# Kernel optimization log

Measured on AMD Instinct MI355X. Metric: run time of the kernel, lower is better.

## Reference

```python
import math
import jax, jax.numpy as jnp
import numpy as np

B, N = 1, 512
C_S, C_Z, H, C, P_Q, P_V = 384, 128, 12, 16, 4, 8
CAT = C_Z * H + C * H + 3 * H * P_V + 1  # 2017


def _apply(t_r, t_t, x):
    # t_r: (b,n,3,3), t_t: (b,n,3), x: (b,3,h,p,n) -> global frame coords
    xg = jnp.einsum('bnij,bjhpn->bihpn', t_r, x)
    return xg + jnp.swapaxes(t_t, 1, 2)[:, :, None, None, :]


def setup_inputs() -> dict:
    key = jax.random.key(0)
    ks = jax.random.split(key, 14)
    f = lambda k, shp: jax.random.normal(k, shp, dtype=jnp.float32)
    return {
        's': f(ks[0], (B, C_S, N)),
        'z': f(ks[1], (B, C_Z, N, N)),
        't_r': f(ks[2], (B, N, 3, 3)),
        't_t': f(ks[3], (B, N, 3)),
        'Wq': f(ks[4], (C * H, C_S)) * 0.02,
        'Wk': f(ks[5], (C * H, C_S)) * 0.02,
        'Wv': f(ks[6], (C * H, C_S)) * 0.02,
        'Wqp': f(ks[7], (3 * H * P_Q, C_S)) * 0.02,
        'Wkp': f(ks[8], (3 * H * P_Q, C_S)) * 0.02,
        'Wvp': f(ks[9], (3 * H * P_V, C_S)) * 0.02,
        'Wb': f(ks[10], (H, C_Z)) * 0.02,
        'gamma': f(ks[11], (H, 1, 1)) * 0.5,
        'Ws': f(ks[12], (C_S, CAT)) * 0.02,
        'bs': jnp.zeros((C_S,), dtype=jnp.float32),
    }


def reference(s, z, t_r, t_t, Wq, Wk, Wv, Wqp, Wkp, Wvp, Wb, gamma, Ws, bs):
    b, _, n = s.shape
    w_c = math.sqrt(2.0 / (9.0 * P_Q))
    w_l = math.sqrt(1.0 / 3.0)

    proj = lambda W: jnp.einsum('oc,bcn->bon', W, s)
    # torch rearrange 'b (c h) i -> b c h i' == reshape(b, c, h, n)
    q = proj(Wq).reshape(b, C, H, n)
    k = proj(Wk).reshape(b, C, H, n)
    v = proj(Wv).reshape(b, C, H, n)
    qp = proj(Wqp).reshape(b, 3, H, P_Q, n)
    kp = proj(Wkp).reshape(b, 3, H, P_Q, n)
    vp = proj(Wvp).reshape(b, 3, H, P_V, n)

    qg = _apply(t_r, t_t, qp)  # (b,3,h,p,n)
    kg = _apply(t_r, t_t, kp)
    diff = qg[..., :, None] - kg[..., None, :]          # (b,3,h,p,n,n)
    dist2 = jnp.sum(diff * diff, axis=(1, 3))           # sum coords + points -> (b,h,n,n)
    tmp = jax.nn.softplus(gamma)[None] * (w_c / 2.0) * dist2

    b_bias = jnp.einsum('hc,bcij->bhij', Wb, z)
    qk = jnp.einsum('bchi,bchj->bhij', q, k) / math.sqrt(C)
    a = jax.nn.softmax(w_l * (qk + b_bias - tmp), axis=-1)  # (b,h,n,n)

    o1 = jnp.einsum('bhij,bcij->bchi', a, z).reshape(b, C_Z * H, n)
    o2 = jnp.einsum('bhij,bchj->bchi', a, v).reshape(b, C * H, n)

    vg = _apply(t_r, t_t, vp)                           # (b,3,h,pv,n)
    o3g = jnp.einsum('bhij,bchpj->bchpi', a, vg)        # (b,3,h,pv,n)
    t_r_inv = jnp.swapaxes(t_r, -1, -2)
    t_t_inv = jnp.einsum('bnij,bnj->bni', -t_r_inv, t_t)
    o3 = _apply(t_r_inv, t_t_inv, o3g).reshape(b, 3 * H * P_V, n)
    o3_norm = jnp.linalg.norm(o3, axis=1, keepdims=True)  # (b,1,n)

    cat = jnp.concatenate([o1, o2, o3, o3_norm], axis=1)  # (b, CAT, n)
    return jnp.einsum('oc,bcn->bon', Ws, cat) + bs[None, :, None]
```

## Files before the change

### kernel.cpp

```cpp
#include <hip/hip_runtime.h>
#include <math.h>

#define N 512
#define H 12
#define CC 16
#define CZ 128
#define CS 384
#define PQ 4
#define PV 8
#define CATR 2017

__global__ __launch_bounds__(256) void k_proj(
    const float* __restrict__ s,
    const float* __restrict__ Wq, const float* __restrict__ Wk, const float* __restrict__ Wv,
    const float* __restrict__ Wqp, const float* __restrict__ Wkp, const float* __restrict__ Wvp,
    float* __restrict__ proj)
{
    __shared__ float Wt[16][33];
    __shared__ float St[32][128];
    int t = threadIdx.x;
    int o0 = blockIdx.x * 16;
    int n0 = blockIdx.y * 128;
    const float* Wsrc; int orow;
    if (o0 < 192)      { Wsrc = Wq;  orow = o0; }
    else if (o0 < 384) { Wsrc = Wk;  orow = o0-192; }
    else if (o0 < 576) { Wsrc = Wv;  orow = o0-384; }
    else if (o0 < 720) { Wsrc = Wqp; orow = o0-576; }
    else if (o0 < 864) { Wsrc = Wkp; orow = o0-720; }
    else               { Wsrc = Wvp; orow = o0-864; }

    int og = t >> 6, nl = t & 63;
    float acc[4][2] = {};
    for (int c0 = 0; c0 < CS; c0 += 32) {
        __syncthreads();
        for (int k = 0; k < 2; k++) {
            int idx = t + k*256;
            int oo = idx >> 5, ccol = idx & 31;
            Wt[oo][ccol] = Wsrc[(orow+oo)*CS + c0 + ccol];
        }
        for (int k = 0; k < 4; k++) {
            int idx = t + k*256;
            int ccr = idx >> 5, nn4 = idx & 31;
            float4 v = *(const float4*)&s[(c0+ccr)*N + n0 + nn4*4];
            *(float4*)&St[ccr][nn4*4] = v;
        }
        __syncthreads();
        for (int kk = 0; kk < 32; kk++) {
            float sv0 = St[kk][nl], sv1 = St[kk][nl+64];
            #pragma unroll
            for (int r = 0; r < 4; r++) {
                float w = Wt[og*4+r][kk];
                acc[r][0] += w * sv0;
                acc[r][1] += w * sv1;
            }
        }
    }
    for (int r = 0; r < 4; r++) {
        int o = o0 + og*4 + r;
        proj[o*N + n0 + nl]      = acc[r][0];
        proj[o*N + n0 + 64 + nl] = acc[r][1];
    }
}

__global__ void k_frames(const float* __restrict__ proj,
                         const float* __restrict__ t_r, const float* __restrict__ t_t,
                         float* __restrict__ qg, float* __restrict__ kg, float* __restrict__ vg)
{
    int gid = blockIdx.x * blockDim.x + threadIdx.x;
    int n = gid & (N-1);
    int hp = gid >> 9;
    if (hp >= 192) return;
    const float* src; float* dst; int rowb, stride;
    if (hp < 48)      { src = proj + 576*N; dst = qg; rowb = hp;    stride = 48; }
    else if (hp < 96) { src = proj + 720*N; dst = kg; rowb = hp-48; stride = 48; }
    else              { src = proj + 864*N; dst = vg; rowb = hp-96; stride = 96; }
    float x0 = src[(rowb + 0*stride)*N + n];
    float x1 = src[(rowb + 1*stride)*N + n];
    float x2 = src[(rowb + 2*stride)*N + n];
    #pragma unroll
    for (int d = 0; d < 3; d++) {
        float r0 = t_r[(n*3+d)*3+0], r1 = t_r[(n*3+d)*3+1], r2 = t_r[(n*3+d)*3+2];
        dst[(rowb + d*stride)*N + n] = r0*x0 + r1*x1 + r2*x2 + t_t[n*3+d];
    }
}

__global__ void k_sq(const float* __restrict__ qg, const float* __restrict__ kg,
                     float* __restrict__ sq_q, float* __restrict__ sq_k)
{
    int gid = blockIdx.x * blockDim.x + threadIdx.x;
    int n = gid & (N-1);
    int sel = gid >> 9;
    int h = sel % H;
    const float* g = (sel < H) ? qg : kg;
    float* outp = (sel < H) ? sq_q : sq_k;
    float acc = 0.f;
    #pragma unroll
    for (int d = 0; d < 3; d++)
        #pragma unroll
        for (int p = 0; p < PQ; p++) {
            float v = g[(size_t)((d*H + h)*PQ + p)*N + n];
            acc += v*v;
        }
    outp[h*N + n] = acc;
}

__global__ __launch_bounds__(256) void k_attn_o1(
    const float* __restrict__ z, const float* __restrict__ proj,
    const float* __restrict__ qg, const float* __restrict__ kg,
    const float* __restrict__ sq_q, const float* __restrict__ sq_k,
    const float* __restrict__ Wb, const float* __restrict__ gamma,
    float* __restrict__ a, float* __restrict__ cat)
{
    __shared__ float als[12*516];
    __shared__ float zls[128*68];
    int i = blockIdx.x;
    int t = threadIdx.x;
    int jl = t & 63;
    int cgu = __builtin_amdgcn_readfirstlane(t >> 6);
    const size_t NN = (size_t)N*N;
    const float w_l  = 0.57735026918962584f;
    const float w_c2 = 0.11785113019775793f;

    float ch[12];
    #pragma unroll
    for (int h = 0; h < 12; h++) {
        float g = gamma[h];
        float sp = (g > 20.f) ? g : log1pf(expf(g));
        ch[h] = sp * w_c2;
    }

    for (int jc = 0; jc < 2; jc++) {
        int j = jc*256 + jl*4;
        float acc[12][4] = {};

        {
            const float* zp = z + (size_t)(cgu*32)*NN + (size_t)i*N + j;
            for (int cc = 0; cc < 32; cc += 8) {
                float4 zb[8];
                #pragma unroll
                for (int u = 0; u < 8; u++)
                    zb[u] = *(const float4*)(zp + (size_t)(cc+u)*NN);
                #pragma unroll
                for (int u = 0; u < 8; u++) {
                    int c = cgu*32 + cc + u;
                    #pragma unroll
                    for (int h = 0; h < 12; h++) {
                        float w = Wb[h*CZ + c];
                        acc[h][0] += w*zb[u].x; acc[h][1] += w*zb[u].y;
                        acc[h][2] += w*zb[u].z; acc[h][3] += w*zb[u].w;
                    }
                }
            }
        }
        {
            const float* q  = proj;
            const float* kk = proj + 192*N;
            #pragma unroll
            for (int cc = 0; cc < 4; cc++) {
                int c = cgu*4 + cc;
                #pragma unroll
                for (int h = 0; h < 12; h++) {
                    int r = c*12 + h;
                    float qv = 0.25f * q[(size_t)r*N + i];
                    float4 k4 = *(const float4*)&kk[(size_t)r*N + j];
                    acc[h][0] += qv*k4.x; acc[h][1] += qv*k4.y;
                    acc[h][2] += qv*k4.z; acc[h][3] += qv*k4.w;
                }
            }
        }
        {
            #pragma unroll
            for (int dd = 0; dd < 3; dd++) {
                int dp = cgu*3 + dd; int d = dp >> 2, p = dp & 3;
                #pragma unroll
                for (int h = 0; h < 12; h++) {
                    int r = (d*12 + h)*4 + p;
                    float qv = 2.f * ch[h] * qg[(size_t)r*N + i];
                    float4 k4 = *(const float4*)&kg[(size_t)r*N + j];
                    acc[h][0] += qv*k4.x; acc[h][1] += qv*k4.y;
                    acc[h][2] += qv*k4.z; acc[h][3] += qv*k4.w;
                }
            }
        }

        __syncthreads();
        float* red = zls;
        if (cgu >= 2) {
            #pragma unroll
            for (int h = 0; h < 12; h++) {
                float4 v; v.x=acc[h][0]; v.y=acc[h][1]; v.z=acc[h][2]; v.w=acc[h][3];
                *(float4*)&red[(h*2 + (cgu-2))*256 + jl*4] = v;
            }
        }
        __syncthreads();
        if (cgu < 2) {
            #pragma unroll
            for (int h = 0; h < 12; h++) {
                float4 o = *(const float4*)&red[(h*2 + cgu)*256 + jl*4];
                acc[h][0] += o.x; acc[h][1] += o.y; acc[h][2] += o.z; acc[h][3] += o.w;
            }
            if (cgu == 1) {
                #pragma unroll
                for (int h = 0; h < 12; h++) {
                    float4 v; v.x=acc[h][0]; v.y=acc[h][1]; v.z=acc[h][2]; v.w=acc[h][3];
                    *(float4*)&red[(h*2 + 1)*256 + jl*4] = v;
                }
            }
        }
        __syncthreads();
        if (cgu == 0) {
            #pragma unroll
            for (int h = 0; h < 12; h++) {
                float4 o = *(const float4*)&red[(h*2 + 1)*256 + jl*4];
                float s0 = sq_q[h*N + i];
                float4 sk = *(const float4*)&sq_k[h*N + j];
                float4 r;
                r.x = w_l*(acc[h][0] + o.x - ch[h]*(s0 + sk.x));
                r.y = w_l*(acc[h][1] + o.y - ch[h]*(s0 + sk.y));
                r.z = w_l*(acc[h][2] + o.z - ch[h]*(s0 + sk.z));
                r.w = w_l*(acc[h][3] + o.w - ch[h]*(s0 + sk.w));
                *(float4*)&als[h*516 + jc*256 + jl*4] = r;
            }
        }
    }
    __syncthreads();

    #pragma unroll
    for (int hh = 0; hh < 3; hh++) {
        int h = cgu*3 + hh;
        float* row = &als[h*516 + jl*8];
        float4 v0 = *(const float4*)row;
        float4 v1 = *(const float4*)(row+4);
        float m = fmaxf(fmaxf(fmaxf(v0.x,v0.y),fmaxf(v0.z,v0.w)),
                        fmaxf(fmaxf(v1.x,v1.y),fmaxf(v1.z,v1.w)));
        for (int s = 32; s > 0; s >>= 1) m = fmaxf(m, __shfl_xor(m, s));
        v0.x = __expf(v0.x-m); v0.y = __expf(v0.y-m);
        v0.z = __expf(v0.z-m); v0.w = __expf(v0.w-m);
        v1.x = __expf(v1.x-m); v1.y = __expf(v1.y-m);
        v1.z = __expf(v1.z-m); v1.w = __expf(v1.w-m);
        float sm = v0.x+v0.y+v0.z+v0.w+v1.x+v1.y+v1.z+v1.w;
        for (int s = 32; s > 0; s >>= 1) sm += __shfl_xor(sm, s);
        float inv = 1.f/sm;
        v0.x*=inv; v0.y*=inv; v0.z*=inv; v0.w*=inv;
        v1.x*=inv; v1.y*=inv; v1.z*=inv; v1.w*=inv;
        *(float4*)row = v0;
        *(float4*)(row+4) = v1;
        float* garow = &a[((size_t)h*N + i)*N + jl*8];
        *(float4*)garow = v0;
        *(float4*)(garow+4) = v1;
    }
    __syncthreads();

    int cg = t & 31, hg = (t>>5)&1, jq = t>>6;
    float acc[4][6] = {};
    for (int jc = 0; jc < 8; jc++) {
        __syncthreads();
        #pragma unroll
        for (int k = 0; k < 8; k++) {
            int idx = t + k*256;
            int c = idx >> 4, j4 = idx & 15;
            *(float4*)&zls[c*68 + j4*4] =
                *(const float4*)&z[((size_t)c*N + i)*N + jc*64 + j4*4];
        }
        __syncthreads();
        #pragma unroll
        for (int s = 0; s < 4; s++) {
            int jo = jq*16 + s*4;
            float4 a4[6];
            #pragma unroll
            for (int hh = 0; hh < 6; hh++)
                a4[hh] = *(const float4*)&als[(hg*6+hh)*516 + jc*64 + jo];
            #pragma unroll
            for (int r = 0; r < 4; r++) {
                float4 zz = *(const float4*)&zls[(cg + 32*r)*68 + jo];
                #pragma unroll
                for (int hh = 0; hh < 6; hh++)
                    acc[r][hh] += zz.x*a4[hh].x + zz.y*a4[hh].y
                                + zz.z*a4[hh].z + zz.w*a4[hh].w;
            }
        }
    }
    __syncthreads();
    if (jq >= 2) {
        float* rb = &zls[((jq-2)*128 + (t & 127))*25];
        #pragma unroll
        for (int r = 0; r < 4; r++)
            #pragma unroll
            for (int hh = 0; hh < 6; hh++) rb[r*6+hh] = acc[r][hh];
    }
    __syncthreads();
    if (jq < 2) {
        const float* rb = &zls[(jq*128 + (t & 127))*25];
        #pragma unroll
        for (int r = 0; r < 4; r++)
            #pragma unroll
            for (int hh = 0; hh < 6; hh++) acc[r][hh] += rb[r*6+hh];
        if (jq == 1) {
            float* rb2 = &als[(t & 63)*25];
            #pragma unroll
            for (int r = 0; r < 4; r++)
                #pragma unroll
                for (int hh = 0; hh < 6; hh++) rb2[r*6+hh] = acc[r][hh];
        }
    }
    __syncthreads();
    if (jq == 0) {
        const float* rb2 = &als[t*25];
        #pragma unroll
        for (int r = 0; r < 4; r++)
            #pragma unroll
            for (int hh = 0; hh < 6; hh++) {
                float v = acc[r][hh] + rb2[r*6+hh];
                int c = cg + 32*r;
                int h = hg*6 + hh;
                cat[(size_t)(c*H + h)*N + i] = v;
            }
    }
}

__global__ __launch_bounds__(256) void k_o2o3g(
    const float* __restrict__ a, const float* __restrict__ proj, const float* __restrict__ vg,
    float* __restrict__ cat, float* __restrict__ o3g)
{
    __shared__ float ats[8*132];
    __shared__ float vts[40*132];
    int h = blockIdx.x, i0 = blockIdx.y*8;
    int t = threadIdx.x;
    int il = t & 7, rg = (t>>3)&7, jq = t>>6;
    const float* v = proj + 384*N;
    float acc[5] = {};
    for (int jc = 0; jc < 4; jc++) {
        __syncthreads();
        {
            int ii = t >> 5, j4 = t & 31;
            *(float4*)&ats[ii*132 + j4*4] =
                *(const float4*)&a[((size_t)h*N + i0+ii)*N + jc*128 + j4*4];
        }
        #pragma unroll
        for (int k = 0; k < 5; k++) {
            int idx = t + k*256;
            int r = idx >> 5, j4 = idx & 31;
            const float* src = (r < 16) ? (v + (size_t)(r*H + h)*N)
                : (vg + (size_t)(((r-16)>>3)*96 + h*PV + ((r-16)&7))*N);
            *(float4*)&vts[r*132 + j4*4] = *(const float4*)&src[jc*128 + j4*4];
        }
        __syncthreads();
        #pragma unroll
        for (int s = 0; s < 8; s++) {
            int jo = jq*32 + s*4;
            float4 a4 = *(const float4*)&ats[il*132 + jo];
            #pragma unroll
            for (int r = 0; r < 5; r++) {
                float4 v4 = *(const float4*)&vts[(rg*5+r)*132 + jo];
                acc[r] += v4.x*a4.x + v4.y*a4.y + v4.z*a4.z + v4.w*a4.w;
            }
        }
    }
    __syncthreads();
    if (jq >= 2) {
        float* rb = &ats[((jq-2)*64 + (t & 63))*5];
        #pragma unroll
        for (int r = 0; r < 5; r++) rb[r] = acc[r];
    }
    __syncthreads();
    if (jq < 2) {
        const float* rb = &ats[(jq*64 + (t & 63))*5];
        #pragma unroll
        for (int r = 0; r < 5; r++) acc[r] += rb[r];
        if (jq == 1) {
            float* rb2 = &ats[640 + (t & 63)*5];
            #pragma unroll
            for (int r = 0; r < 5; r++) rb2[r] = acc[r];
        }
    }
    __syncthreads();
    if (jq == 0) {
        const float* rb2 = &ats[640 + t*5];
        #pragma unroll
        for (int r = 0; r < 5; r++) {
            float val = acc[r] + rb2[r];
            int row = rg*5 + r;
            if (row < 16) cat[(size_t)(1536 + row*H + h)*N + i0 + il] = val;
            else { int rr = row - 16;
                   o3g[(size_t)((rr>>3)*96 + h*PV + (rr&7))*N + i0 + il] = val; }
        }
    }
}

__global__ void k_o3(const float* __restrict__ o3g,
                     const float* __restrict__ t_r, const float* __restrict__ t_t,
                     float* __restrict__ cat)
{
    int gid = blockIdx.x*blockDim.x + threadIdx.x;
    int i = gid & (N-1), hp = gid >> 9;
    if (hp >= 96) return;
    float x0 = o3g[(size_t)(0*96 + hp)*N + i] - t_t[i*3+0];
    float x1 = o3g[(size_t)(1*96 + hp)*N + i] - t_t[i*3+1];
    float x2 = o3g[(size_t)(2*96 + hp)*N + i] - t_t[i*3+2];
    #pragma unroll
    for (int d = 0; d < 3; d++) {
        float o = t_r[(i*3+0)*3+d]*x0 + t_r[(i*3+1)*3+d]*x1 + t_r[(i*3+2)*3+d]*x2;
        cat[(size_t)(1728 + d*96 + hp)*N + i] = o;
    }
}

__global__ void k_norm(float* __restrict__ cat)
{
    int i = blockIdx.x*blockDim.x + threadIdx.x;
    if (i >= N) return;
    float acc = 0.f;
    for (int r = 0; r < 288; r++) {
        float v = cat[(size_t)(1728+r)*N + i];
        acc += v*v;
    }
    cat[(size_t)2016*N + i] = sqrtf(acc);
}

__global__ __launch_bounds__(256) void k_final(
    const float* __restrict__ Ws, const float* __restrict__ bs,
    const float* __restrict__ cat, float* __restrict__ out)
{
    __shared__ float Wt[16*33];
    __shared__ float Ct[32*66];
    int o0 = blockIdx.x*16, n0 = blockIdx.y*64;
    int ks = blockIdx.z;
    int kbeg = ks*505, kend = min(CATR, kbeg+505);
    int t = threadIdx.x;
    int og = t >> 6, nl = t & 63;
    float acc[4] = {};
    for (int c0 = kbeg; c0 < kend; c0 += 32) {
        __syncthreads();
        for (int k = 0; k < 2; k++) {
            int idx = t + k*256;
            int oo = idx >> 5, ccol = idx & 31;
            int c = c0 + ccol;
            Wt[oo*33 + ccol] = (c < kend) ? Ws[(size_t)(o0+oo)*CATR + c] : 0.f;
        }
        for (int k = 0; k < 4; k++) {
            int idx = t + k*256;
            int ccr = idx >> 5, j2 = idx & 31;
            int c = c0 + ccr;
            float2 vv; vv.x = 0.f; vv.y = 0.f;
            if (c < kend) vv = *(const float2*)&cat[(size_t)c*N + n0 + j2*2];
            *(float2*)&Ct[ccr*66 + j2*2] = vv;
        }
        __syncthreads();
        int klim = min(32, kend - c0);
        for (int kk = 0; kk < klim; kk++) {
            float cv = Ct[kk*66 + nl];
            #pragma unroll
            for (int r = 0; r < 4; r++)
                acc[r] += Wt[(og*4+r)*33 + kk] * cv;
        }
    }
    #pragma unroll
    for (int r = 0; r < 4; r++) {
        int o = o0 + og*4 + r;
        float val = acc[r];
        if (ks == 0) val += bs[o];
        atomicAdd(&out[(size_t)o*N + n0 + nl], val);
    }
}

extern "C" void kernel_launch(void* const* d_in, const int* in_sizes, int n_in,
                              void* d_out, int out_size, void* d_ws, size_t ws_size,
                              hipStream_t stream)
{
    const float* s     = (const float*)d_in[0];
    const float* z     = (const float*)d_in[1];
    const float* t_r   = (const float*)d_in[2];
    const float* t_t   = (const float*)d_in[3];
    const float* Wq    = (const float*)d_in[4];
    const float* Wk    = (const float*)d_in[5];
    const float* Wv    = (const float*)d_in[6];
    const float* Wqp   = (const float*)d_in[7];
    const float* Wkp   = (const float*)d_in[8];
    const float* Wvp   = (const float*)d_in[9];
    const float* Wb    = (const float*)d_in[10];
    const float* gamma = (const float*)d_in[11];
    const float* Ws    = (const float*)d_in[12];
    const float* bs    = (const float*)d_in[13];
    float* out = (float*)d_out;

    float* ws   = (float*)d_ws;
    float* proj = ws;
    float* qg   = proj + 1152*N;
    float* kg   = qg   + 144*N;
    float* vg   = kg   + 144*N;
    float* sq_q = vg   + 288*N;
    float* sq_k = sq_q + H*N;
    float* o3g  = sq_k + H*N;
    float* a    = o3g  + 288*N;
    float* cat  = a    + (size_t)H*N*N;

    k_proj   <<<dim3(72,4),   256, 0, stream>>>(s, Wq, Wk, Wv, Wqp, Wkp, Wvp, proj);
    k_frames <<<384,          256, 0, stream>>>(proj, t_r, t_t, qg, kg, vg);
    k_sq     <<<48,           256, 0, stream>>>(qg, kg, sq_q, sq_k);
    k_attn_o1<<<512,          256, 0, stream>>>(z, proj, qg, kg, sq_q, sq_k, Wb, gamma, a, cat);
    k_o2o3g  <<<dim3(12,64),  256, 0, stream>>>(a, proj, vg, cat, o3g);
    k_o3     <<<192,          256, 0, stream>>>(o3g, t_r, t_t, cat);
    k_norm   <<<2,            256, 0, stream>>>(cat);
    hipMemsetAsync(out, 0, (size_t)CS*N*sizeof(float), stream);
    k_final  <<<dim3(24,8,4), 256, 0, stream>>>(Ws, bs, cat, out);
}
```

Measured before the change: 410.4 us.

## Split fused attention kernel into bias, softmax and o1 kernels with i-major logits

Replaces the single per-row kernel that computed logits, softmax and the z-weighted output into three kernels: a bias/logit kernel tiled over (i,j) blocks, a standalone softmax over a padded i-major logits buffer, and an o1 kernel that keeps attention rows in registers and streams z tiles through shared memory. The attention matrix is now stored as [i][h][j] with padded rows, and k_o2o3g reads that layout. The aim is better parallelism and occupancy than the 512-block fused kernel with its heavy shared memory and cross-wave reductions. In exchange, z is read twice from global memory and the logits take an extra global round trip.

```diff
diff --git a/kernel.cpp b/kernel.cpp
--- a/kernel.cpp
+++ b/kernel.cpp
@@ -9,6 +9,8 @@
 #define PQ 4
 #define PV 8
 #define CATR 2017
+#define ATROW 520
+#define ATPL  (H*ATROW)
 
 __global__ __launch_bounds__(256) void k_proj(
     const float* __restrict__ s,
@@ -104,22 +106,36 @@
     outp[h*N + n] = acc;
 }
 
-__global__ __launch_bounds__(256) void k_attn_o1(
+__global__ __launch_bounds__(128) void k_bias(
     const float* __restrict__ z, const float* __restrict__ proj,
     const float* __restrict__ qg, const float* __restrict__ kg,
     const float* __restrict__ sq_q, const float* __restrict__ sq_k,
     const float* __restrict__ Wb, const float* __restrict__ gamma,
-    float* __restrict__ a, float* __restrict__ cat)
-{
-    __shared__ float als[12*516];
-    __shared__ float zls[128*68];
-    int i = blockIdx.x;
+    float* __restrict__ a_t)
+{
+    __shared__ float q_ls[192*4];
+    __shared__ float qg_ls[144*4];
+    __shared__ float sqq_ls[12*4];
     int t = threadIdx.x;
-    int jl = t & 63;
-    int cgu = __builtin_amdgcn_readfirstlane(t >> 6);
+    int ii = t >> 5;
+    int jj = t & 31;
+    int i0 = blockIdx.x * 4;
+    int j0 = blockIdx.y * 128;
+    int i = i0 + ii;
+    int j4 = j0 + jj*4;
     const size_t NN = (size_t)N*N;
     const float w_l  = 0.57735026918962584f;
     const float w_c2 = 0.11785113019775793f;
+
+    for (int kk = 0; kk < 6; kk++) {
+        int idx = kk*128 + t;
+        if (idx < 768) { int r = idx >> 2, i2 = idx & 3; q_ls[idx] = proj[r*N + i0 + i2]; }
+    }
+    for (int kk = 0; kk < 5; kk++) {
+        int idx = kk*128 + t;
+        if (idx < 576) { int r = idx >> 2, i2 = idx & 3; qg_ls[idx] = qg[r*N + i0 + i2]; }
+    }
+    if (t < 48) { int r = t >> 2, i2 = t & 3; sqq_ls[t] = sq_q[r*N + i0 + i2]; }
 
     float ch[12];
     #pragma unroll
@@ -128,109 +144,68 @@
         float sp = (g > 20.f) ? g : log1pf(expf(g));
         ch[h] = sp * w_c2;
     }
-
-    for (int jc = 0; jc < 2; jc++) {
-        int j = jc*256 + jl*4;
-        float acc[12][4] = {};
-
-        {
-            const float* zp = z + (size_t)(cgu*32)*NN + (size_t)i*N + j;
-            for (int cc = 0; cc < 32; cc += 8) {
-                float4 zb[8];
-                #pragma unroll
-                for (int u = 0; u < 8; u++)
-                    zb[u] = *(const float4*)(zp + (size_t)(cc+u)*NN);
-                #pragma unroll
-                for (int u = 0; u < 8; u++) {
-                    int c = cgu*32 + cc + u;
-                    #pragma unroll
-                    for (int h = 0; h < 12; h++) {
-                        float w = Wb[h*CZ + c];
-                        acc[h][0] += w*zb[u].x; acc[h][1] += w*zb[u].y;
-                        acc[h][2] += w*zb[u].z; acc[h][3] += w*zb[u].w;
-                    }
-                }
+    __syncthreads();
+
+    float4 acc[12];
+    #pragma unroll
+    for (int h = 0; h < 12; h++) { acc[h].x=0.f; acc[h].y=0.f; acc[h].z=0.f; acc[h].w=0.f; }
+    for (int cb = 0; cb < CZ; cb += 8) {
+        float4 zb[8];
+        #pragma unroll
+        for (int u = 0; u < 8; u++)
+            zb[u] = *(const float4*)&z[(size_t)(cb+u)*NN + (size_t)i*N + j4];
+        #pragma unroll
+        for (int u = 0; u < 8; u++) {
+            int c = cb + u;
+            #pragma unroll
+            for (int h = 0; h < 12; h++) {
+                float w = Wb[h*CZ + c];
+                acc[h].x += w*zb[u].x; acc[h].y += w*zb[u].y;
+                acc[h].z += w*zb[u].z; acc[h].w += w*zb[u].w;
             }
         }
-        {
-            const float* q  = proj;
-            const float* kk = proj + 192*N;
-            #pragma unroll
-            for (int cc = 0; cc < 4; cc++) {
-                int c = cgu*4 + cc;
-                #pragma unroll
-                for (int h = 0; h < 12; h++) {
-                    int r = c*12 + h;
-                    float qv = 0.25f * q[(size_t)r*N + i];
-                    float4 k4 = *(const float4*)&kk[(size_t)r*N + j];
-                    acc[h][0] += qv*k4.x; acc[h][1] += qv*k4.y;
-                    acc[h][2] += qv*k4.z; acc[h][3] += qv*k4.w;
-                }
-            }
-        }
-        {
-            #pragma unroll
-            for (int dd = 0; dd < 3; dd++) {
-                int dp = cgu*3 + dd; int d = dp >> 2, p = dp & 3;
-                #pragma unroll
-                for (int h = 0; h < 12; h++) {
-                    int r = (d*12 + h)*4 + p;
-                    float qv = 2.f * ch[h] * qg[(size_t)r*N + i];
-                    float4 k4 = *(const float4*)&kg[(size_t)r*N + j];
-                    acc[h][0] += qv*k4.x; acc[h][1] += qv*k4.y;
-                    acc[h][2] += qv*k4.z; acc[h][3] += qv*k4.w;
-                }
-            }
-        }
-
-        __syncthreads();
-        float* red = zls;
-        if (cgu >= 2) {
-            #pragma unroll
-            for (int h = 0; h < 12; h++) {
-                float4 v; v.x=acc[h][0]; v.y=acc[h][1]; v.z=acc[h][2]; v.w=acc[h][3];
-                *(float4*)&red[(h*2 + (cgu-2))*256 + jl*4] = v;
-            }
-        }
-        __syncthreads();
-        if (cgu < 2) {
-            #pragma unroll
-            for (int h = 0; h < 12; h++) {
-                float4 o = *(const float4*)&red[(h*2 + cgu)*256 + jl*4];
-                acc[h][0] += o.x; acc[h][1] += o.y; acc[h][2] += o.z; acc[h][3] += o.w;
-            }
-            if (cgu == 1) {
-                #pragma unroll
-                for (int h = 0; h < 12; h++) {
-                    float4 v; v.x=acc[h][0]; v.y=acc[h][1]; v.z=acc[h][2]; v.w=acc[h][3];
-                    *(float4*)&red[(h*2 + 1)*256 + jl*4] = v;
-                }
-            }
-        }
-        __syncthreads();
-        if (cgu == 0) {
-            #pragma unroll
-            for (int h = 0; h < 12; h++) {
-                float4 o = *(const float4*)&red[(h*2 + 1)*256 + jl*4];
-                float s0 = sq_q[h*N + i];
-                float4 sk = *(const float4*)&sq_k[h*N + j];
-                float4 r;
-                r.x = w_l*(acc[h][0] + o.x - ch[h]*(s0 + sk.x));
-                r.y = w_l*(acc[h][1] + o.y - ch[h]*(s0 + sk.y));
-                r.z = w_l*(acc[h][2] + o.z - ch[h]*(s0 + sk.z));
-                r.w = w_l*(acc[h][3] + o.w - ch[h]*(s0 + sk.w));
-                *(float4*)&als[h*516 + jc*256 + jl*4] = r;
-            }
-        }
-    }
-    __syncthreads();
-
+    }
+
+    const float* kmat = proj + 192*N;
+    #pragma unroll
+    for (int h = 0; h < 12; h++) {
+        float4 qk; qk.x=0.f; qk.y=0.f; qk.z=0.f; qk.w=0.f;
+        #pragma unroll
+        for (int c = 0; c < 16; c++) {
+            int r = c*12 + h;
+            float  qs = q_ls[r*4 + ii];
+            float4 kv = *(const float4*)&kmat[(size_t)r*N + j4];
+            qk.x += qs*kv.x; qk.y += qs*kv.y; qk.z += qs*kv.z; qk.w += qs*kv.w;
+        }
+        float4 g4; g4.x=0.f; g4.y=0.f; g4.z=0.f; g4.w=0.f;
+        #pragma unroll
+        for (int dp = 0; dp < 12; dp++) {
+            int r = ((dp>>2)*12 + h)*4 + (dp&3);
+            float  qgs = qg_ls[r*4 + ii];
+            float4 kgv = *(const float4*)&kg[(size_t)r*N + j4];
+            g4.x += qgs*kgv.x; g4.y += qgs*kgv.y; g4.z += qgs*kgv.z; g4.w += qgs*kgv.w;
+        }
+        float  sqq = sqq_ls[h*4 + ii];
+        float4 sk  = *(const float4*)&sq_k[h*N + j4];
+        float4 l;
+        l.x = w_l*(acc[h].x + 0.25f*qk.x + ch[h]*(2.f*g4.x - sqq - sk.x));
+        l.y = w_l*(acc[h].y + 0.25f*qk.y + ch[h]*(2.f*g4.y - sqq - sk.y));
+        l.z = w_l*(acc[h].z + 0.25f*qk.z + ch[h]*(2.f*g4.z - sqq - sk.z));
+        l.w = w_l*(acc[h].w + 0.25f*qk.w + ch[h]*(2.f*g4.w - sqq - sk.w));
+        *(float4*)&a_t[(size_t)i*ATPL + h*ATROW + j4] = l;
+    }
+}
+
+__global__ __launch_bounds__(256) void k_softmax_t(float* __restrict__ a_t)
+{
+    int i = blockIdx.x;
+    int w = threadIdx.x >> 6, l = threadIdx.x & 63;
     #pragma unroll
     for (int hh = 0; hh < 3; hh++) {
-        int h = cgu*3 + hh;
-        float* row = &als[h*516 + jl*8];
+        int h = w*3 + hh;
+        float* row = a_t + (size_t)i*ATPL + h*ATROW + l*8;
         float4 v0 = *(const float4*)row;
-        float4 v1 = *(const float4*)(row+4);
+        float4 v1 = *(const float4*)(row + 4);
         float m = fmaxf(fmaxf(fmaxf(v0.x,v0.y),fmaxf(v0.z,v0.w)),
                         fmaxf(fmaxf(v1.x,v1.y),fmaxf(v1.z,v1.w)));
         for (int s = 32; s > 0; s >>= 1) m = fmaxf(m, __shfl_xor(m, s));
@@ -245,81 +220,68 @@
         v1.x*=inv; v1.y*=inv; v1.z*=inv; v1.w*=inv;
         *(float4*)row = v0;
         *(float4*)(row+4) = v1;
-        float* garow = &a[((size_t)h*N + i)*N + jl*8];
-        *(float4*)garow = v0;
-        *(float4*)(garow+4) = v1;
-    }
-    __syncthreads();
-
-    int cg = t & 31, hg = (t>>5)&1, jq = t>>6;
-    float acc[4][6] = {};
-    for (int jc = 0; jc < 8; jc++) {
-        __syncthreads();
-        #pragma unroll
-        for (int k = 0; k < 8; k++) {
-            int idx = t + k*256;
-            int c = idx >> 4, j4 = idx & 15;
-            *(float4*)&zls[c*68 + j4*4] =
-                *(const float4*)&z[((size_t)c*N + i)*N + jc*64 + j4*4];
-        }
-        __syncthreads();
-        #pragma unroll
-        for (int s = 0; s < 4; s++) {
-            int jo = jq*16 + s*4;
-            float4 a4[6];
-            #pragma unroll
-            for (int hh = 0; hh < 6; hh++)
-                a4[hh] = *(const float4*)&als[(hg*6+hh)*516 + jc*64 + jo];
-            #pragma unroll
-            for (int r = 0; r < 4; r++) {
-                float4 zz = *(const float4*)&zls[(cg + 32*r)*68 + jo];
-                #pragma unroll
-                for (int hh = 0; hh < 6; hh++)
-                    acc[r][hh] += zz.x*a4[hh].x + zz.y*a4[hh].y
-                                + zz.z*a4[hh].z + zz.w*a4[hh].w;
+    }
+}
+
+__global__ __launch_bounds__(192) void k_o1_t(
+    const float* __restrict__ z, const float* __restrict__ a_t, float* __restrict__ cat)
+{
+    __shared__ float zls[4*2*512];
+    int t = threadIdx.x;
+    int ii = t / 96;
+    int rem = t - ii*96;
+    int h  = rem >> 3;
+    int js = rem & 7;
+    int c0 = blockIdx.x * 32;
+    int i0 = blockIdx.y * 2;
+    const size_t NN = (size_t)N*N;
+
+    float4 areg[16];
+    #pragma unroll
+    for (int m = 0; m < 16; m++)
+        areg[m] = *(const float4*)&a_t[(size_t)(i0+ii)*ATPL + h*ATROW + js*4 + m*32];
+
+    float acc[32];
+    #pragma unroll
+    for (int c = 0; c < 32; c++) acc[c] = 0.f;
+
+    #pragma unroll
+    for (int cb = 0; cb < 32; cb += 4) {
+        __syncthreads();
+        for (int kk = 0; kk < 6; kk++) {
+            int idx = kk*192 + t;
+            if (idx < 1024) {
+                int cu = idx >> 8, i2 = (idx >> 7) & 1, jf = (idx & 127) * 4;
+                *(float4*)&zls[cu*1024 + i2*512 + jf] =
+                    *(const float4*)&z[(size_t)(c0+cb+cu)*NN + (size_t)(i0+i2)*N + jf];
             }
         }
-    }
-    __syncthreads();
-    if (jq >= 2) {
-        float* rb = &zls[((jq-2)*128 + (t & 127))*25];
-        #pragma unroll
-        for (int r = 0; r < 4; r++)
-            #pragma unroll
-            for (int hh = 0; hh < 6; hh++) rb[r*6+hh] = acc[r][hh];
-    }
-    __syncthreads();
-    if (jq < 2) {
-        const float* rb = &zls[(jq*128 + (t & 127))*25];
-        #pragma unroll
-        for (int r = 0; r < 4; r++)
-            #pragma unroll
-            for (int hh = 0; hh < 6; hh++) acc[r][hh] += rb[r*6+hh];
-        if (jq == 1) {
-            float* rb2 = &als[(t & 63)*25];
-            #pragma unroll
-            for (int r = 0; r < 4; r++)
-                #pragma unroll
-                for (int hh = 0; hh < 6; hh++) rb2[r*6+hh] = acc[r][hh];
-        }
-    }
-    __syncthreads();
-    if (jq == 0) {
-        const float* rb2 = &als[t*25];
-        #pragma unroll
-        for (int r = 0; r < 4; r++)
-            #pragma unroll
-            for (int hh = 0; hh < 6; hh++) {
-                float v = acc[r][hh] + rb2[r*6+hh];
-                int c = cg + 32*r;
-                int h = hg*6 + hh;
-                cat[(size_t)(c*H + h)*N + i] = v;
+        __syncthreads();
+        #pragma unroll
+        for (int u = 0; u < 4; u++) {
+            float s = 0.f;
+            #pragma unroll
+            for (int m = 0; m < 16; m++) {
+                float4 zz = *(const float4*)&zls[u*1024 + ii*512 + js*4 + m*32];
+                s += zz.x*areg[m].x + zz.y*areg[m].y + zz.z*areg[m].z + zz.w*areg[m].w;
             }
+            acc[cb+u] += s;
+        }
+    }
+
+    #pragma unroll
+    for (int c = 0; c < 32; c++) {
+        float v = acc[c];
+        v += __shfl_xor(v, 1);
+        v += __shfl_xor(v, 2);
+        v += __shfl_xor(v, 4);
+        if (js == 0)
+            cat[(size_t)((c0+c)*H + h)*N + i0 + ii] = v;
     }
 }
 
 __global__ __launch_bounds__(256) void k_o2o3g(
-    const float* __restrict__ a, const float* __restrict__ proj, const float* __restrict__ vg,
+    const float* __restrict__ a_t, const float* __restrict__ proj, const float* __restrict__ vg,
     float* __restrict__ cat, float* __restrict__ o3g)
 {
     __shared__ float ats[8*132];
@@ -334,7 +296,7 @@
         {
             int ii = t >> 5, j4 = t & 31;
             *(float4*)&ats[ii*132 + j4*4] =
-                *(const float4*)&a[((size_t)h*N + i0+ii)*N + jc*128 + j4*4];
+                *(const float4*)&a_t[(size_t)(i0+ii)*ATPL + h*ATROW + jc*128 + j4*4];
         }
         #pragma unroll
         for (int k = 0; k < 5; k++) {
@@ -490,16 +452,18 @@
     float* sq_q = vg   + 288*N;
     float* sq_k = sq_q + H*N;
     float* o3g  = sq_k + H*N;
-    float* a    = o3g  + 288*N;
-    float* cat  = a    + (size_t)H*N*N;
-
-    k_proj   <<<dim3(72,4),   256, 0, stream>>>(s, Wq, Wk, Wv, Wqp, Wkp, Wvp, proj);
-    k_frames <<<384,          256, 0, stream>>>(proj, t_r, t_t, qg, kg, vg);
-    k_sq     <<<48,           256, 0, stream>>>(qg, kg, sq_q, sq_k);
-    k_attn_o1<<<512,          256, 0, stream>>>(z, proj, qg, kg, sq_q, sq_k, Wb, gamma, a, cat);
-    k_o2o3g  <<<dim3(12,64),  256, 0, stream>>>(a, proj, vg, cat, o3g);
-    k_o3     <<<192,          256, 0, stream>>>(o3g, t_r, t_t, cat);
-    k_norm   <<<2,            256, 0, stream>>>(cat);
+    float* a_t  = o3g  + 288*N;
+    float* cat  = a_t  + (size_t)N*ATPL;
+
+    k_proj     <<<dim3(72,4),   256, 0, stream>>>(s, Wq, Wk, Wv, Wqp, Wkp, Wvp, proj);
+    k_frames   <<<384,          256, 0, stream>>>(proj, t_r, t_t, qg, kg, vg);
+    k_sq       <<<48,           256, 0, stream>>>(qg, kg, sq_q, sq_k);
+    k_bias     <<<dim3(128,4),  128, 0, stream>>>(z, proj, qg, kg, sq_q, sq_k, Wb, gamma, a_t);
+    k_softmax_t<<<512,          256, 0, stream>>>(a_t);
+    k_o1_t     <<<dim3(4,256),  192, 0, stream>>>(z, a_t, cat);
+    k_o2o3g    <<<dim3(12,64),  256, 0, stream>>>(a_t, proj, vg, cat, o3g);
+    k_o3       <<<192,          256, 0, stream>>>(o3g, t_r, t_t, cat);
+    k_norm     <<<2,            256, 0, stream>>>(cat);
     hipMemsetAsync(out, 0, (size_t)CS*N*sizeof(float), stream);
-    k_final  <<<dim3(24,8,4), 256, 0, stream>>>(Ws, bs, cat, out);
-}
+    k_final    <<<dim3(24,8,4), 256, 0, stream>>>(Ws, bs, cat, out);
+}
```

Result: slower. 1.525 ms (+271.5%).
